# Optimization experiments

Hardware: AMD Instinct MI355X
Metric: run time of the kernel (lower is better)

Reference implementation:

```python
import jax, jax.numpy as jnp
import numpy as np

N_CLASSES = 12
IMG_SIZE = 512
BATCH = 8

CURV_MAX = jnp.array([1.2261, 1.1558, 1.1161, 1.1195, 2.7202, 2.3714,
                      1.7055, 3.2717, 2.6716, 5.0418, 0.4293], dtype=jnp.float32)


def setup_inputs() -> dict:
    key = jax.random.key(0)
    soft_anatomy = jax.random.normal(key, (BATCH, N_CLASSES, IMG_SIZE, IMG_SIZE), dtype=jnp.float32)
    return {"soft_anatomy": soft_anatomy}


def reference(soft_anatomy):
    nc1 = N_CLASSES - 1  # 11 layer channels
    pred_mask = soft_anatomy[:, :nc1]                      # [B, 11, H, W]
    sm = jax.nn.softmax(pred_mask, axis=2)                 # softmax over height (dim 2)
    lsm = jax.nn.log_softmax(pred_mask, axis=2)
    B, C, H, W = sm.shape

    # position mask: row index broadcast over width/channels
    pos = jnp.arange(H, dtype=sm.dtype)[None, None, :, None]  # [1,1,H,1]

    # expected layer position per column: [B, 11, W]
    layer_positions = jnp.sum(sm * pos, axis=2)

    # std deviations around layer positions: [B, 11, W]
    std_deviations = jnp.sqrt(
        jnp.sum(sm * (pos - layer_positions[:, :, None, :]) ** 2, axis=2))

    # topology violations between adjacent layers: [B, 10, W]
    topology_violations = jax.nn.relu(layer_positions[:, :-1] - layer_positions[:, 1:])

    # neighbour (continuity) diff along width: [B, 11, W-1]
    continuity_violations = jnp.abs(
        (jnp.roll(layer_positions, 1, axis=2) - layer_positions)[..., 1:])

    # curvature via depthwise conv1d with sobel [-1,0..0,1] and laplace [1,0..0,-2,0..0,1]
    # (kernel length 11, replicate pad 5 -> same width). torch conv1d is cross-correlation:
    #   first[w]  = -x[w] + x[w+10]
    #   second[w] =  x[w] - 2*x[w+5] + x[w+10]
    PAD = 5
    lpp = jnp.pad(layer_positions, ((0, 0), (0, 0), (PAD, PAD)), mode='edge')
    first_order = lpp[..., 10:] - lpp[..., :-10]
    second_order = lpp[..., :-10] - 2.0 * lpp[..., 5:-5] + lpp[..., 10:]
    curvature = second_order / jnp.power(1.0 + first_order ** 2, 1.5)
    curvature_diffs = jnp.abs(curvature) - CURV_MAX[None, :, None]  # curv_max broadcast over W

    # topological_engine_1d: new[i] = max(new[i-1], lp[i]) == cumulative max over class dim
    correct_layer_positions = jax.lax.cummax(layer_positions, axis=1)

    # cumulative mask: ones channel + cumsum over height -> [B, 12, H, W]
    cum = jnp.cumsum(sm, axis=2)
    ones = jnp.ones((B, 1, H, W), dtype=sm.dtype)
    cm = jnp.concatenate([ones, cum], axis=1)

    # topological_engine_2d: y[idx] = relu(c[idx] + y[idx-1] - 1), idx = 2..n_classes-1
    def step(carry, c):
        y = jax.nn.relu(c + carry - 1.0)
        return y, y

    _, ys = jax.lax.scan(step, cm[:, 1], jnp.moveaxis(cm[:, 2:], 1, 0))
    top_correct = jnp.concatenate([cm[:, :2], jnp.moveaxis(ys, 0, 1)], axis=1)  # [B,12,H,W]

    # separate_masks: forward diff in place; last channel unchanged
    clean_masks = jnp.concatenate(
        [top_correct[:, :-1] - top_correct[:, 1:], top_correct[:, -1:]], axis=1)

    return (lsm, correct_layer_positions, clean_masks,
            std_deviations, topology_violations, continuity_violations, curvature_diffs)
```

## Files before the change

kernel.cpp:

```cpp
#include <hip/hip_runtime.h>

#define BB 8
#define NC 12
#define NC1 11
#define HH 512
#define WW 512
#define NCH 32
#define HC 16
#define WT 32
#define XLD 34

static constexpr size_t CH = (size_t)HH * WW;

static constexpr size_t OFF_LSM   = 0;
static constexpr size_t OFF_CLP   = (size_t)BB * NC1 * CH;
static constexpr size_t OFF_CLEAN = OFF_CLP + (size_t)BB * NC1 * WW;
static constexpr size_t OFF_STD   = OFF_CLEAN + (size_t)BB * NC * CH;
static constexpr size_t OFF_TOPO  = OFF_STD + (size_t)BB * NC1 * WW;
static constexpr size_t OFF_CONT  = OFF_TOPO + (size_t)BB * (NC1 - 1) * WW;
static constexpr size_t OFF_CURV  = OFF_CONT + (size_t)BB * NC1 * (WW - 1);

static constexpr size_t WS_BASE = 0;
static constexpr size_t WS_LP   = WS_BASE + (size_t)BB * NC1 * NCH * WW;

__global__ __launch_bounds__(512) void ks_stats(const float* __restrict__ in,
                                                float* __restrict__ ws,
                                                float* __restrict__ out) {
    const int t  = threadIdx.x;
    const int wt = blockIdx.x, c = blockIdx.y, b = blockIdx.z;
    const int bc = b * NC1 + c;
    const int w0 = wt * WT;

    __shared__ float xs[HH][XLD];
    __shared__ float cs[NCH][WT];
    __shared__ float pP[16][WT];
    __shared__ float pQ[16][WT];
    __shared__ float lgS[WT];

    {
        const int w2 = t & 15, r = t >> 4;
        const float* p = in + (size_t)(b * NC + c) * CH + (size_t)r * WW + w0 + 2 * w2;
#pragma unroll
        for (int i = 0; i < 16; ++i) {
            float2 v = *(const float2*)(p + (size_t)(i * 32) * WW);
            xs[r + 32 * i][2 * w2]     = v.x;
            xs[r + 32 * i][2 * w2 + 1] = v.y;
        }
    }
    __syncthreads();

    {
        const int w = t & 31, q = t >> 5;
        float P = 0.f, Q = 0.f;
#pragma unroll
        for (int j = 0; j < 2; ++j) {
            float E = 0.f;
#pragma unroll
            for (int i = 0; i < HC; ++i) {
                const int h = q * 32 + j * HC + i;
                const float e = expf(xs[h][w]);
                const float hf = (float)h;
                E += e; P += hf * e; Q += hf * hf * e;
            }
            cs[q * 2 + j][w] = E;
        }
        pP[q][w] = P; pQ[q][w] = Q;
    }
    __syncthreads();

    if (t < WT) {
        const int w = t;
        float S = 0.f;
#pragma unroll
        for (int ch = 0; ch < NCH; ++ch) S += cs[ch][w];
        const float inv = 1.f / S;
        float run = 0.f;
#pragma unroll
        for (int ch = 0; ch < NCH; ++ch) {
            const float e = cs[ch][w];
            cs[ch][w] = run * inv;
            run += e;
        }
        float P = 0.f, Q = 0.f;
#pragma unroll
        for (int q = 0; q < 16; ++q) { P += pP[q][w]; Q += pQ[q][w]; }
        const float lp = P * inv;
        float var = Q * inv - lp * lp; if (var < 0.f) var = 0.f;
        lgS[w] = logf(S);
        const size_t o = (size_t)bc * WW + w0 + w;
        ws[WS_LP + o] = lp;
        out[OFF_STD + o] = sqrtf(var);
    }
    __syncthreads();

    {
        const int w = t & 31, chg = t >> 5;
#pragma unroll
        for (int j = 0; j < 2; ++j) {
            const int ch = chg * 2 + j;
            ws[WS_BASE + ((size_t)bc * NCH + ch) * WW + w0 + w] = cs[ch][w];
        }
    }
    {
        const int w2 = t & 15, r = t >> 4;
        const float l0 = lgS[2 * w2], l1 = lgS[2 * w2 + 1];
        float* lo = out + OFF_LSM + (size_t)bc * CH + (size_t)r * WW + w0 + 2 * w2;
#pragma unroll
        for (int i = 0; i < 16; ++i) {
            const int h = r + 32 * i;
            float2 v = make_float2(xs[h][2 * w2] - l0, xs[h][2 * w2 + 1] - l1);
            *(float2*)(lo + (size_t)(i * 32) * WW) = v;
        }
    }
}

__global__ __launch_bounds__(256) void kc_clean(const float* __restrict__ ws,
                                                float* __restrict__ out) {
    const int t = threadIdx.x;
    const int wh = blockIdx.x, chunk = blockIdx.y, b = blockIdx.z;
    const int w = wh * 256 + t;

    float cum[NC1];
#pragma unroll
    for (int c = 0; c < NC1; ++c)
        cum[c] = ws[WS_BASE + (((size_t)(b * NC1 + c)) * NCH + chunk) * WW + w];

    const float* lsm = out + OFF_LSM + (size_t)b * NC1 * CH + (size_t)(chunk * HC) * WW + w;
    float* cln = out + OFF_CLEAN + (size_t)b * NC * CH + (size_t)(chunk * HC) * WW + w;

    for (int i = 0; i < HC; ++i) {
        const size_t ho = (size_t)i * WW;
        float s[NC1];
#pragma unroll
        for (int c = 0; c < NC1; ++c)
            s[c] = expf(lsm[(size_t)c * CH + ho]);
#pragma unroll
        for (int c = 0; c < NC1; ++c)
            cum[c] += s[c];
        float tc = cum[0];
        cln[ho] = 1.f - tc;
#pragma unroll
        for (int k = 1; k < NC1; ++k) {
            const float t2 = fmaxf(cum[k] + tc - 1.f, 0.f);
            cln[(size_t)k * CH + ho] = tc - t2;
            tc = t2;
        }
        cln[(size_t)NC1 * CH + ho] = tc;
    }

    if (chunk != 0) return;
    const float CM[NC1] = {1.2261f, 1.1558f, 1.1161f, 1.1195f, 2.7202f, 2.3714f,
                           1.7055f, 3.2717f, 2.6716f, 5.0418f, 0.4293f};
    const float* lp = ws + WS_LP;
    const int wm = (w - 5 < 0) ? 0 : w - 5;
    const int wp = (w + 5 > WW - 1) ? WW - 1 : w + 5;
    float m = 0.f, prev = 0.f;
    for (int c = 0; c < NC1; ++c) {
        const size_t rb = (size_t)(b * NC1 + c) * WW;
        const float lv = lp[rb + w];
        m = (c == 0) ? lv : fmaxf(m, lv);
        out[OFF_CLP + rb + w] = m;
        if (c > 0)
            out[OFF_TOPO + (size_t)(b * (NC1 - 1) + (c - 1)) * WW + w] = fmaxf(prev - lv, 0.f);
        prev = lv;
        if (w < WW - 1) {
            const float nxt = lp[rb + w + 1];
            out[OFF_CONT + (size_t)(b * NC1 + c) * (WW - 1) + w] = fabsf(lv - nxt);
        }
        const float a  = lp[rb + wm];
        const float bb = lp[rb + wp];
        const float fo = bb - a;
        const float so = a - 2.f * lv + bb;
        const float bs = 1.f + fo * fo;
        out[OFF_CURV + rb + w] = fabsf(so / (bs * sqrtf(bs))) - CM[c];
    }
}

extern "C" void kernel_launch(void* const* d_in, const int* in_sizes, int n_in,
                              void* d_out, int out_size, void* d_ws, size_t ws_size,
                              hipStream_t stream) {
    const float* in = (const float*)d_in[0];
    float* out = (float*)d_out;
    float* ws = (float*)d_ws;

    hipLaunchKernelGGL(ks_stats, dim3(16, NC1, BB), dim3(512), 0, stream, in, ws, out);
    hipLaunchKernelGGL(kc_clean, dim3(2, NCH, BB), dim3(256), 0, stream, ws, out);
}
```

Measured before the change: 81.31 us.

## Split stats into partial-sum and reduce kernels, compute log-softmax in final pass

Replaces the shared-memory-staged stats kernel with three kernels. The first computes per-chunk exp, h·exp and h²·exp partial sums using float4 loads. The second reduces them per column into prefix cumsums, inverse sum, log-sum, layer position and std. The final kernel reads the input again instead of the lsm output, writes log-softmax and the clean masks there with nontemporal stores, and so drops the first kernel's second full-tensor write pass. The cost is reading the input twice, more workspace traffic for the P/Q partials, and an extra launch.

```diff
diff --git a/kernel.cpp b/kernel.cpp
--- a/kernel.cpp
+++ b/kernel.cpp
@@ -7,8 +7,7 @@
 #define WW 512
 #define NCH 32
 #define HC 16
-#define WT 32
-#define XLD 34
+#define NBC (BB*NC1)
 
 static constexpr size_t CH = (size_t)HH * WW;
 
@@ -20,132 +19,113 @@
 static constexpr size_t OFF_CONT  = OFF_TOPO + (size_t)BB * (NC1 - 1) * WW;
 static constexpr size_t OFF_CURV  = OFF_CONT + (size_t)BB * NC1 * (WW - 1);
 
-static constexpr size_t WS_BASE = 0;
-static constexpr size_t WS_LP   = WS_BASE + (size_t)BB * NC1 * NCH * WW;
+static constexpr size_t WS_E    = 0;
+static constexpr size_t WS_P    = (size_t)NBC * NCH * WW;
+static constexpr size_t WS_Q    = 2 * WS_P;
+static constexpr size_t WS_INV  = 3 * WS_P;
+static constexpr size_t WS_LOG  = WS_INV + (size_t)NBC * WW;
+static constexpr size_t WS_LP   = WS_LOG + (size_t)NBC * WW;
 
-__global__ __launch_bounds__(512) void ks_stats(const float* __restrict__ in,
-                                                float* __restrict__ ws,
-                                                float* __restrict__ out) {
-    const int t  = threadIdx.x;
-    const int wt = blockIdx.x, c = blockIdx.y, b = blockIdx.z;
-    const int bc = b * NC1 + c;
-    const int w0 = wt * WT;
+__global__ __launch_bounds__(512) void k1_partials(const float* __restrict__ in,
+                                                   float* __restrict__ ws) {
+    const int w4 = threadIdx.x & 127;
+    const int cg = threadIdx.x >> 7;
+    const int chunk = blockIdx.x * 4 + cg;
+    const int bc = blockIdx.y;
+    const int b = bc / NC1, c = bc % NC1;
 
-    __shared__ float xs[HH][XLD];
-    __shared__ float cs[NCH][WT];
-    __shared__ float pP[16][WT];
-    __shared__ float pQ[16][WT];
-    __shared__ float lgS[WT];
-
-    {
-        const int w2 = t & 15, r = t >> 4;
-        const float* p = in + (size_t)(b * NC + c) * CH + (size_t)r * WW + w0 + 2 * w2;
+    const float* p = in + ((size_t)(b * NC + c) * HH + (size_t)chunk * HC) * WW + 4 * w4;
+    float4 E = make_float4(0.f, 0.f, 0.f, 0.f);
+    float4 P = E, Q = E;
 #pragma unroll
-        for (int i = 0; i < 16; ++i) {
-            float2 v = *(const float2*)(p + (size_t)(i * 32) * WW);
-            xs[r + 32 * i][2 * w2]     = v.x;
-            xs[r + 32 * i][2 * w2 + 1] = v.y;
-        }
+    for (int i = 0; i < HC; ++i) {
+        const float4 x = *(const float4*)(p + (size_t)i * WW);
+        const float h = (float)(chunk * HC + i);
+        const float ex = expf(x.x), ey = expf(x.y), ez = expf(x.z), ew = expf(x.w);
+        E.x += ex; E.y += ey; E.z += ez; E.w += ew;
+        P.x += h * ex; P.y += h * ey; P.z += h * ez; P.w += h * ew;
+        Q.x += h * h * ex; Q.y += h * h * ey; Q.z += h * h * ez; Q.w += h * h * ew;
     }
-    __syncthreads();
-
-    {
-        const int w = t & 31, q = t >> 5;
-        float P = 0.f, Q = 0.f;
-#pragma unroll
-        for (int j = 0; j < 2; ++j) {
-            float E = 0.f;
-#pragma unroll
-            for (int i = 0; i < HC; ++i) {
-                const int h = q * 32 + j * HC + i;
-                const float e = expf(xs[h][w]);
-                const float hf = (float)h;
-                E += e; P += hf * e; Q += hf * hf * e;
-            }
-            cs[q * 2 + j][w] = E;
-        }
-        pP[q][w] = P; pQ[q][w] = Q;
-    }
-    __syncthreads();
-
-    if (t < WT) {
-        const int w = t;
-        float S = 0.f;
-#pragma unroll
-        for (int ch = 0; ch < NCH; ++ch) S += cs[ch][w];
-        const float inv = 1.f / S;
-        float run = 0.f;
-#pragma unroll
-        for (int ch = 0; ch < NCH; ++ch) {
-            const float e = cs[ch][w];
-            cs[ch][w] = run * inv;
-            run += e;
-        }
-        float P = 0.f, Q = 0.f;
-#pragma unroll
-        for (int q = 0; q < 16; ++q) { P += pP[q][w]; Q += pQ[q][w]; }
-        const float lp = P * inv;
-        float var = Q * inv - lp * lp; if (var < 0.f) var = 0.f;
-        lgS[w] = logf(S);
-        const size_t o = (size_t)bc * WW + w0 + w;
-        ws[WS_LP + o] = lp;
-        out[OFF_STD + o] = sqrtf(var);
-    }
-    __syncthreads();
-
-    {
-        const int w = t & 31, chg = t >> 5;
-#pragma unroll
-        for (int j = 0; j < 2; ++j) {
-            const int ch = chg * 2 + j;
-            ws[WS_BASE + ((size_t)bc * NCH + ch) * WW + w0 + w] = cs[ch][w];
-        }
-    }
-    {
-        const int w2 = t & 15, r = t >> 4;
-        const float l0 = lgS[2 * w2], l1 = lgS[2 * w2 + 1];
-        float* lo = out + OFF_LSM + (size_t)bc * CH + (size_t)r * WW + w0 + 2 * w2;
-#pragma unroll
-        for (int i = 0; i < 16; ++i) {
-            const int h = r + 32 * i;
-            float2 v = make_float2(xs[h][2 * w2] - l0, xs[h][2 * w2 + 1] - l1);
-            *(float2*)(lo + (size_t)(i * 32) * WW) = v;
-        }
-    }
+    const size_t o = ((size_t)bc * NCH + chunk) * WW + 4 * w4;
+    *(float4*)(ws + WS_E + o) = E;
+    *(float4*)(ws + WS_P + o) = P;
+    *(float4*)(ws + WS_Q + o) = Q;
 }
 
-__global__ __launch_bounds__(256) void kc_clean(const float* __restrict__ ws,
-                                                float* __restrict__ out) {
+__global__ __launch_bounds__(512) void k2_reduce(float* __restrict__ ws,
+                                                 float* __restrict__ out) {
+    const int w = threadIdx.x;
+    const int bc = blockIdx.x;
+
+    const size_t base0 = (size_t)bc * NCH * WW + w;
+    float Ee[NCH];
+    float S = 0.f, P = 0.f, Q = 0.f;
+#pragma unroll
+    for (int k = 0; k < NCH; ++k) {
+        const float e = ws[WS_E + base0 + (size_t)k * WW];
+        Ee[k] = e;
+        S += e;
+        P += ws[WS_P + base0 + (size_t)k * WW];
+        Q += ws[WS_Q + base0 + (size_t)k * WW];
+    }
+    const float inv = 1.f / S;
+    float pre = 0.f;
+#pragma unroll
+    for (int k = 0; k < NCH; ++k) {
+        ws[WS_E + base0 + (size_t)k * WW] = pre * inv;
+        pre += Ee[k];
+    }
+    const float lp = P * inv;
+    float var = Q * inv - lp * lp;
+    if (var < 0.f) var = 0.f;
+
+    const size_t o = (size_t)bc * WW + w;
+    ws[WS_INV + o] = inv;
+    ws[WS_LOG + o] = logf(S);
+    ws[WS_LP + o]  = lp;
+    out[OFF_STD + o] = sqrtf(var);
+}
+
+__global__ __launch_bounds__(256) void k4_main(const float* __restrict__ in,
+                                               const float* __restrict__ ws,
+                                               float* __restrict__ out) {
     const int t = threadIdx.x;
     const int wh = blockIdx.x, chunk = blockIdx.y, b = blockIdx.z;
     const int w = wh * 256 + t;
 
-    float cum[NC1];
+    float cum[NC1], inv[NC1], lgs[NC1];
 #pragma unroll
-    for (int c = 0; c < NC1; ++c)
-        cum[c] = ws[WS_BASE + (((size_t)(b * NC1 + c)) * NCH + chunk) * WW + w];
+    for (int c = 0; c < NC1; ++c) {
+        const size_t bc = (size_t)(b * NC1 + c);
+        cum[c] = ws[WS_E + (bc * NCH + chunk) * WW + w];
+        inv[c] = ws[WS_INV + bc * WW + w];
+        lgs[c] = ws[WS_LOG + bc * WW + w];
+    }
 
-    const float* lsm = out + OFF_LSM + (size_t)b * NC1 * CH + (size_t)(chunk * HC) * WW + w;
+    const float* ip = in + (size_t)b * NC * CH + (size_t)(chunk * HC) * WW + w;
+    float* lsm = out + OFF_LSM + (size_t)b * NC1 * CH + (size_t)(chunk * HC) * WW + w;
     float* cln = out + OFF_CLEAN + (size_t)b * NC * CH + (size_t)(chunk * HC) * WW + w;
 
     for (int i = 0; i < HC; ++i) {
         const size_t ho = (size_t)i * WW;
-        float s[NC1];
+        float x[NC1];
 #pragma unroll
         for (int c = 0; c < NC1; ++c)
-            s[c] = expf(lsm[(size_t)c * CH + ho]);
+            x[c] = ip[(size_t)c * CH + ho];
 #pragma unroll
-        for (int c = 0; c < NC1; ++c)
-            cum[c] += s[c];
+        for (int c = 0; c < NC1; ++c) {
+            cum[c] += expf(x[c]) * inv[c];
+            __builtin_nontemporal_store(x[c] - lgs[c], lsm + (size_t)c * CH + ho);
+        }
         float tc = cum[0];
-        cln[ho] = 1.f - tc;
+        __builtin_nontemporal_store(1.f - tc, cln + ho);
 #pragma unroll
         for (int k = 1; k < NC1; ++k) {
             const float t2 = fmaxf(cum[k] + tc - 1.f, 0.f);
-            cln[(size_t)k * CH + ho] = tc - t2;
+            __builtin_nontemporal_store(tc - t2, cln + (size_t)k * CH + ho);
             tc = t2;
         }
-        cln[(size_t)NC1 * CH + ho] = tc;
+        __builtin_nontemporal_store(tc, cln + (size_t)NC1 * CH + ho);
     }
 
     if (chunk != 0) return;
@@ -183,6 +163,7 @@
     float* out = (float*)d_out;
     float* ws = (float*)d_ws;
 
-    hipLaunchKernelGGL(ks_stats, dim3(16, NC1, BB), dim3(512), 0, stream, in, ws, out);
-    hipLaunchKernelGGL(kc_clean, dim3(2, NCH, BB), dim3(256), 0, stream, ws, out);
+    hipLaunchKernelGGL(k1_partials, dim3(NCH / 4, NBC), dim3(512), 0, stream, in, ws);
+    hipLaunchKernelGGL(k2_reduce, dim3(NBC), dim3(512), 0, stream, ws, out);
+    hipLaunchKernelGGL(k4_main, dim3(2, NCH, BB), dim3(256), 0, stream, in, ws, out);
 }
```

New measurement: 78.40 us. 1.04x faster.
